# Performance work log

Hardware: AMD Instinct MI355X
Metric: run time of the kernel (lower is better)

## Reference

```python
import jax, jax.numpy as jnp
import numpy as np

HIDDEN = 1024
NUM_HEAD = 16
HEAD_DIM = HIDDEN // NUM_HEAD
B, S = 2, 2048


def setup_inputs() -> dict:
    key = jax.random.key(0)
    ks = jax.random.split(key, 9)
    scale = 1.0 / np.sqrt(HIDDEN)
    X = jax.random.normal(ks[0], (B, S, HIDDEN), dtype=jnp.float32)
    # causal mask, broadcastable over heads: [B, 1, S, S]
    causal = jnp.tril(jnp.ones((S, S), dtype=jnp.int32))
    mask = jnp.broadcast_to(causal[None, None, :, :], (B, 1, S, S))
    Wq = jax.random.normal(ks[1], (HIDDEN, HIDDEN), dtype=jnp.float32) * scale
    bq = jnp.zeros((HIDDEN,), dtype=jnp.float32)
    Wk = jax.random.normal(ks[2], (HIDDEN, HIDDEN), dtype=jnp.float32) * scale
    bk = jnp.zeros((HIDDEN,), dtype=jnp.float32)
    Wv = jax.random.normal(ks[3], (HIDDEN, HIDDEN), dtype=jnp.float32) * scale
    bv = jnp.zeros((HIDDEN,), dtype=jnp.float32)
    Wo = jax.random.normal(ks[4], (HIDDEN, HIDDEN), dtype=jnp.float32) * scale
    bo = jnp.zeros((HIDDEN,), dtype=jnp.float32)
    return {"X": X, "mask": mask, "Wq": Wq, "bq": bq, "Wk": Wk, "bk": bk,
            "Wv": Wv, "bv": bv, "Wo": Wo, "bo": bo}


def reference(X, mask, Wq, bq, Wk, bk, Wv, bv, Wo, bo):
    bsz, seq_len, _ = X.shape
    # Q/K/V projections (torch Linear: x @ W.T + b; here W stored as [in, out])
    Q = X @ Wq + bq
    K = X @ Wk + bk
    V = X @ Wv + bv
    # [B, H, S, D]
    Q = Q.reshape(bsz, seq_len, NUM_HEAD, HEAD_DIM).transpose(0, 2, 1, 3)
    K = K.reshape(bsz, seq_len, NUM_HEAD, HEAD_DIM).transpose(0, 2, 1, 3)
    V = V.reshape(bsz, seq_len, NUM_HEAD, HEAD_DIM).transpose(0, 2, 1, 3)
    # scores: [B, H, S, S]
    scores = jnp.einsum('bhqd,bhkd->bhqk', Q, K) / jnp.sqrt(
        jnp.asarray(HEAD_DIM, dtype=X.dtype))
    scores = jnp.where(mask == 0, jnp.asarray(-jnp.inf, dtype=scores.dtype), scores)
    # dropout (rate=0.0) is identity; softmax over keys
    attn = jax.nn.softmax(scores, axis=-1)
    out = jnp.einsum('bhqk,bhkd->bhqd', attn, V)
    out = out.transpose(0, 2, 1, 3).reshape(bsz, seq_len, HIDDEN)
    return out @ Wo + bo
```

## Files before the change

### kernel.cpp

```cpp
#include <hip/hip_runtime.h>
#include <stdint.h>

#define HID 1024
#define SEQ 2048
#define NB 2
#define NH 16
#define HD 64
#define MROWS 4096

typedef float f32x4 __attribute__((ext_vector_type(4)));
typedef short s16x4 __attribute__((ext_vector_type(4)));
typedef short s16x8 __attribute__((ext_vector_type(8)));

#define MFMA16(a, b, c) __builtin_amdgcn_mfma_f32_16x16x32_bf16((a), (b), (c), 0, 0, 0)

#define GLOAD_LDS16(gp, lp)                                                    \
  __builtin_amdgcn_global_load_lds(                                            \
      (const __attribute__((address_space(1))) unsigned int*)(gp),             \
      (__attribute__((address_space(3))) unsigned int*)(lp), 16, 0, 0)

__device__ __forceinline__ short f2bf(float x) {
  uint32_t u = __builtin_bit_cast(uint32_t, x);
  u += 0x7fffu + ((u >> 16) & 1u);
  return (short)(u >> 16);
}

__global__ __launch_bounds__(256) void cast_x_kernel(const float* __restrict__ src,
                                                     short* __restrict__ dst) {
  const size_t i = (size_t)blockIdx.x * 256 + threadIdx.x;
  const float* s = src + i * 8;
  f32x4 a = *(const f32x4*)(s);
  f32x4 b = *(const f32x4*)(s + 4);
  s16x8 o;
  o[0] = f2bf(a[0]); o[1] = f2bf(a[1]); o[2] = f2bf(a[2]); o[3] = f2bf(a[3]);
  o[4] = f2bf(b[0]); o[5] = f2bf(b[1]); o[6] = f2bf(b[2]); o[7] = f2bf(b[3]);
  *(s16x8*)(dst + i * 8) = o;
}

__global__ __launch_bounds__(256) void transpose_cast4_kernel(
    const float* __restrict__ w0, const float* __restrict__ w1,
    const float* __restrict__ w2, const float* __restrict__ w3,
    short* __restrict__ dstall) {
  __shared__ float t[32][33];
  const int z = blockIdx.z;
  const float* src = (z == 0) ? w0 : (z == 1) ? w1 : (z == 2) ? w2 : w3;
  short* dst = dstall + ((size_t)z << 20);
  const int tx = threadIdx.x & 31, ty = threadIdx.x >> 5;
  const int r0 = blockIdx.y * 32, c0 = blockIdx.x * 32;
#pragma unroll
  for (int i = 0; i < 4; i++)
    t[ty + i * 8][tx] = src[(size_t)(r0 + ty + i * 8) * HID + c0 + tx];
  __syncthreads();
#pragma unroll
  for (int i = 0; i < 4; i++)
    dst[(size_t)(c0 + ty + i * 8) * HID + r0 + tx] = f2bf(t[tx][ty + i * 8]);
}

template <int EPI>
__global__ __launch_bounds__(256) void gemm_bf16(
    const short* __restrict__ A, const short* __restrict__ Bt,
    const float* __restrict__ b0, const float* __restrict__ b1,
    const float* __restrict__ b2, short* __restrict__ Qb, short* __restrict__ Kg,
    short* __restrict__ Vg, float* __restrict__ Out) {
  __shared__ char lds[16384];
  const int tid = threadIdx.x;
  const int w = tid >> 6, l = tid & 63, lg = l >> 4, ln = l & 15;
  const int wm = w >> 1, wn = w & 1;
  const int m0 = blockIdx.y * 128, n0 = blockIdx.x * 128;

  f32x4 acc[4][4];
#pragma unroll
  for (int i = 0; i < 4; i++)
#pragma unroll
    for (int j = 0; j < 4; j++) acc[i][j] = f32x4{0.f, 0.f, 0.f, 0.f};

  for (int k0 = 0; k0 < 1024; k0 += 32) {
    __syncthreads();
#pragma unroll
    for (int i = 0; i < 2; i++) {
      const int chunk = (w * 2 + i) * 64 + l;
      const int row = chunk >> 2;
      const int cs = (chunk & 3) ^ (row & 3);
      GLOAD_LDS16(A + (size_t)(m0 + row) * 1024 + k0 + cs * 8,
                  lds + (w * 2 + i) * 1024);
      GLOAD_LDS16(Bt + (size_t)(n0 + row) * 1024 + k0 + cs * 8,
                  lds + 8192 + (w * 2 + i) * 1024);
    }
    __syncthreads();

    s16x8 af[4], bfr[4];
#pragma unroll
    for (int mi = 0; mi < 4; mi++) {
      const int row = wm * 64 + mi * 16 + ln;
      af[mi] = *(const s16x8*)(lds + row * 64 + ((lg ^ (row & 3)) * 16));
    }
#pragma unroll
    for (int ni = 0; ni < 4; ni++) {
      const int row = wn * 64 + ni * 16 + ln;
      bfr[ni] = *(const s16x8*)(lds + 8192 + row * 64 + ((lg ^ (row & 3)) * 16));
    }
#pragma unroll
    for (int mi = 0; mi < 4; mi++)
#pragma unroll
      for (int ni = 0; ni < 4; ni++)
        acc[mi][ni] = MFMA16(af[mi], bfr[ni], acc[mi][ni]);
  }

#pragma unroll
  for (int ni = 0; ni < 4; ni++) {
    const int c = n0 + wn * 64 + ni * 16 + ln;
    if (EPI == 0) {
      const int mat = c >> 10, cc = c & 1023, hh = cc >> 6, d = cc & 63;
      const float* bp = (mat == 0) ? b0 : (mat == 1) ? b1 : b2;
      const float bias = bp[cc];
#pragma unroll
      for (int mi = 0; mi < 4; mi++) {
#pragma unroll
        for (int r = 0; r < 4; r++) {
          const int m = m0 + wm * 64 + mi * 16 + lg * 4 + r;
          const int bb = m >> 11, s = m & 2047;
          const short v = f2bf(acc[mi][ni][r] + bias);
          const size_t bh = (size_t)(bb * 16 + hh);
          if (mat == 0) {
            Qb[(bh * SEQ + s) * HD + d] = v;
          } else if (mat == 1) {
            const int tile = s >> 6, rr = s & 63;
            Kg[bh * (SEQ * HD) + tile * 4096 + rr * 64 +
               ((((d >> 3) ^ (rr & 7)) << 3) | (d & 7))] = v;
          } else {
            const int sp = (s & ~31) | ((s & 12) << 1) | (((s >> 4) & 1) << 2) |
                           (s & 3);
            const int tile = sp >> 6, kp = sp & 63;
            Vg[bh * (SEQ * HD) + tile * 4096 + d * 64 +
               ((((kp >> 3) ^ (d & 7)) << 3) | (kp & 7))] = v;
          }
        }
      }
    } else {
      const float bias = b0[c];
#pragma unroll
      for (int mi = 0; mi < 4; mi++)
#pragma unroll
        for (int r = 0; r < 4; r++) {
          const int m = m0 + wm * 64 + mi * 16 + lg * 4 + r;
          Out[(size_t)m * 1024 + c] = acc[mi][ni][r] + bias;
        }
    }
  }
}


__device__ __forceinline__ void stage_tile(const short* Kt, const short* Vt,
                                           int t, char* buf, int w, int l) {
  const char* src = (w < 2) ? ((const char*)(Kt + (size_t)t * 4096) + (w & 1) * 4096)
                            : ((const char*)(Vt + (size_t)t * 4096) + (w & 1) * 4096);
  char* dst = buf + ((w < 2) ? 0 : 8192) + (w & 1) * 4096;
#pragma unroll
  for (int j = 0; j < 4; j++)
    GLOAD_LDS16(src + j * 1024 + l * 16, dst + j * 1024);
}

template <bool MASK>
__device__ __forceinline__ void softmax_pv(f32x4 st[4], const s16x8 vf[2][4],
                                           f32x4 o[4], float& m2, float& l_run,
                                           int k0, int qrow, int lg) {
  const float SC = 0.18033688011112042f;
  float p[4][4];
  float pmax = -3e38f;
#pragma unroll
  for (int mt = 0; mt < 4; mt++)
#pragma unroll
    for (int r = 0; r < 4; r++) {
      float v = st[mt][r] * SC;
      if (MASK) {
        const int key = k0 + mt * 16 + lg * 4 + r;
        if (key > qrow) v = -3e38f;
      }
      p[mt][r] = v;
      pmax = fmaxf(pmax, v);
    }
  pmax = fmaxf(pmax, __shfl_xor(pmax, 16));
  pmax = fmaxf(pmax, __shfl_xor(pmax, 32));
  const float m_new = fmaxf(m2, pmax);
  const float corr = exp2f(m2 - m_new);
  float psum = 0.f;
#pragma unroll
  for (int mt = 0; mt < 4; mt++)
#pragma unroll
    for (int r = 0; r < 4; r++) {
      const float e = exp2f(p[mt][r] - m_new);
      p[mt][r] = e;
      psum += e;
    }
  psum += __shfl_xor(psum, 16);
  psum += __shfl_xor(psum, 32);
  l_run = l_run * corr + psum;
  m2 = m_new;
#pragma unroll
  for (int i = 0; i < 4; i++) o[i] *= corr;

  s16x8 pf[2];
#pragma unroll
  for (int s = 0; s < 2; s++)
#pragma unroll
    for (int h = 0; h < 2; h++)
#pragma unroll
      for (int r = 0; r < 4; r++) pf[s][h * 4 + r] = f2bf(p[s * 2 + h][r]);
#pragma unroll
  for (int s = 0; s < 2; s++)
#pragma unroll
    for (int vmt = 0; vmt < 4; vmt++)
      o[vmt] = MFMA16(vf[s][vmt], pf[s], o[vmt]);
}

template <bool MASK>
__device__ __forceinline__ void compute_tile(const char* cbuf, const s16x8& qf0,
                                             const s16x8& qf1, int k0, int qrow,
                                             int lg, int ln, float& m2,
                                             float& l_run, f32x4 o[4]) {
  const int x = ln & 7;
  f32x4 st[4];
#pragma unroll
  for (int mt = 0; mt < 4; mt++) {
    const char* rowp = cbuf + (mt * 16 + ln) * 128;
    const s16x8 k0f = *(const s16x8*)(rowp + ((lg ^ x) * 16));
    const s16x8 k1f = *(const s16x8*)(rowp + (((4 + lg) ^ x) * 16));
    st[mt] = f32x4{0.f, 0.f, 0.f, 0.f};
    st[mt] = MFMA16(k0f, qf0, st[mt]);
    st[mt] = MFMA16(k1f, qf1, st[mt]);
  }
  s16x8 vf[2][4];
#pragma unroll
  for (int s = 0; s < 2; s++)
#pragma unroll
    for (int vmt = 0; vmt < 4; vmt++)
      vf[s][vmt] = *(const s16x8*)(cbuf + 8192 + (vmt * 16 + ln) * 128 +
                                   (((s * 4 + lg) ^ x) * 16));
  softmax_pv<MASK>(st, vf, o, m2, l_run, k0, qrow, lg);
}

__device__ __forceinline__ void attn_group_pass(const short* Kt, const short* Vt,
                                                const short* __restrict__ Qb,
                                                short* __restrict__ Ob, int bh,
                                                int G, int w, int l, char* lds) {
  const int lg = l >> 4, ln = l & 15;
  const int qrow = G * 64 + w * 16 + ln;
  const short* Qp = Qb + ((size_t)bh * SEQ + qrow) * HD;
  const s16x8 qf0 = *(const s16x8*)(Qp + lg * 8);
  const s16x8 qf1 = *(const s16x8*)(Qp + 32 + lg * 8);

  float m2 = -3e38f, l_run = 0.f;
  f32x4 o[4];
#pragma unroll
  for (int i = 0; i < 4; i++) o[i] = f32x4{0.f, 0.f, 0.f, 0.f};

  const int nt = G + 1;
  stage_tile(Kt, Vt, 0, lds, w, l);
  for (int t = 0; t < nt - 1; ++t) {
    stage_tile(Kt, Vt, t + 1, lds + ((t + 1) & 1) * 16384, w, l);
    asm volatile("s_waitcnt vmcnt(4)" ::: "memory");
    __builtin_amdgcn_s_barrier();
    __builtin_amdgcn_sched_barrier(0);
    compute_tile<false>(lds + (t & 1) * 16384, qf0, qf1, t * 64, qrow, lg, ln,
                        m2, l_run, o);
    __builtin_amdgcn_s_barrier();
    __builtin_amdgcn_sched_barrier(0);
  }
  asm volatile("s_waitcnt vmcnt(0)" ::: "memory");
  __builtin_amdgcn_s_barrier();
  __builtin_amdgcn_sched_barrier(0);
  compute_tile<true>(lds + ((nt - 1) & 1) * 16384, qf0, qf1, (nt - 1) * 64, qrow,
                     lg, ln, m2, l_run, o);
  __builtin_amdgcn_s_barrier();
  __builtin_amdgcn_sched_barrier(0);

  const float inv = 1.0f / l_run;
  const int bb = bh >> 4, hh = bh & 15;
  const size_t orow = (size_t)(bb * SEQ + qrow) * HID + hh * HD;
#pragma unroll
  for (int mt = 0; mt < 4; mt++) {
    s16x4 ov;
#pragma unroll
    for (int r = 0; r < 4; r++) ov[r] = f2bf(o[mt][r] * inv);
    *(s16x4*)(Ob + orow + mt * 16 + lg * 4) = ov;
  }
}

__global__ __launch_bounds__(256) void attn_kernel(const short* __restrict__ Qb,
                                                   const short* __restrict__ Kg,
                                                   const short* __restrict__ Vg,
                                                   short* __restrict__ Ob) {
  __shared__ char lds[32768];
  const int bid = blockIdx.x;
  const int L = (bid & 7) * 64 + (bid >> 3);
  const int bh = L >> 4, g = L & 15;
  const int w = threadIdx.x >> 6, l = threadIdx.x & 63;
  const short* Kt = Kg + (size_t)bh * (SEQ * HD);
  const short* Vt = Vg + (size_t)bh * (SEQ * HD);
  attn_group_pass(Kt, Vt, Qb, Ob, bh, g, w, l, lds);
  attn_group_pass(Kt, Vt, Qb, Ob, bh, 31 - g, w, l, lds);
}

extern "C" void kernel_launch(void* const* d_in, const int* in_sizes, int n_in,
                              void* d_out, int out_size, void* d_ws,
                              size_t ws_size, hipStream_t stream) {
  const float* X = (const float*)d_in[0];
  const float* Wq = (const float*)d_in[2];
  const float* bq = (const float*)d_in[3];
  const float* Wk = (const float*)d_in[4];
  const float* bk = (const float*)d_in[5];
  const float* Wv = (const float*)d_in[6];
  const float* bv = (const float*)d_in[7];
  const float* Wo = (const float*)d_in[8];
  const float* bo = (const float*)d_in[9];
  float* out = (float*)d_out;

  char* ws = (char*)d_ws;
  short* Xb = (short*)(ws);
  short* Wtall = (short*)(ws + (8u << 20));
  short* Qb = (short*)(ws + (16u << 20));
  short* Kg = (short*)(ws + (24u << 20));
  short* Vg = (short*)(ws + (32u << 20));
  short* Ob = (short*)(ws + (40u << 20));
  short* Wto = Wtall + (3u << 20);

  cast_x_kernel<<<2048, 256, 0, stream>>>(X, Xb);
  transpose_cast4_kernel<<<dim3(32, 32, 4), 256, 0, stream>>>(Wq, Wk, Wv, Wo,
                                                              Wtall);

  gemm_bf16<0><<<dim3(24, 32), 256, 0, stream>>>(Xb, Wtall, bq, bk, bv, Qb, Kg,
                                                 Vg, nullptr);
  attn_kernel<<<512, 256, 0, stream>>>(Qb, Kg, Vg, Ob);
  gemm_bf16<1><<<dim3(8, 32), 256, 0, stream>>>(Ob, Wto, bo, nullptr, nullptr,
                                                nullptr, nullptr, nullptr, out);
}
```

Measured before the change: 238.0 us.

## Fuse prep kernels, fold softmax scale into Q, lazy rescale, MFMA row-sum

Merges the X cast and weight transpose into one prep launch, applies the softmax scale to Q in the projection epilogue, and skips the online-softmax rescale unless the max grows by more than a threshold. Row sums are computed with an MFMA against a ones vector and P is packed with a packed bf16 convert instruction. The output projection GEMM uses a smaller 64-row tile for a larger grid. Lazy rescaling lets exponent values grow up to 2^8 before correction, and the row sum now uses bf16-rounded probabilities.

```diff
diff --git a/kernel.cpp b/kernel.cpp
--- a/kernel.cpp
+++ b/kernel.cpp
@@ -11,6 +11,7 @@
 typedef float f32x4 __attribute__((ext_vector_type(4)));
 typedef short s16x4 __attribute__((ext_vector_type(4)));
 typedef short s16x8 __attribute__((ext_vector_type(8)));
+typedef uint32_t u32x4 __attribute__((ext_vector_type(4)));
 
 #define MFMA16(a, b, c) __builtin_amdgcn_mfma_f32_16x16x32_bf16((a), (b), (c), 0, 0, 0)
 
@@ -25,26 +26,36 @@
   return (short)(u >> 16);
 }
 
-__global__ __launch_bounds__(256) void cast_x_kernel(const float* __restrict__ src,
-                                                     short* __restrict__ dst) {
-  const size_t i = (size_t)blockIdx.x * 256 + threadIdx.x;
-  const float* s = src + i * 8;
-  f32x4 a = *(const f32x4*)(s);
-  f32x4 b = *(const f32x4*)(s + 4);
-  s16x8 o;
-  o[0] = f2bf(a[0]); o[1] = f2bf(a[1]); o[2] = f2bf(a[2]); o[3] = f2bf(a[3]);
-  o[4] = f2bf(b[0]); o[5] = f2bf(b[1]); o[6] = f2bf(b[2]); o[7] = f2bf(b[3]);
-  *(s16x8*)(dst + i * 8) = o;
-}
-
-__global__ __launch_bounds__(256) void transpose_cast4_kernel(
-    const float* __restrict__ w0, const float* __restrict__ w1,
-    const float* __restrict__ w2, const float* __restrict__ w3,
-    short* __restrict__ dstall) {
+__device__ __forceinline__ uint32_t cvtpk(float lo, float hi) {
+  uint32_t r;
+  asm("v_cvt_pk_bf16_f32 %0, %1, %2" : "=v"(r) : "v"(lo), "v"(hi));
+  return r;
+}
+
+__global__ __launch_bounds__(256) void prep_kernel(
+    const float* __restrict__ X, const float* __restrict__ w0,
+    const float* __restrict__ w1, const float* __restrict__ w2,
+    const float* __restrict__ w3, short* __restrict__ Xb,
+    short* __restrict__ Wtall) {
+  const int z = blockIdx.z;
+  if (z == 4) {
+    const size_t i = ((size_t)blockIdx.y * 32 + blockIdx.x) * 256 + threadIdx.x;
+    const float* s = X + i * 16;
+    short* d = Xb + i * 16;
+#pragma unroll
+    for (int h = 0; h < 2; h++) {
+      f32x4 a = *(const f32x4*)(s + h * 8);
+      f32x4 b = *(const f32x4*)(s + h * 8 + 4);
+      s16x8 o;
+      o[0] = f2bf(a[0]); o[1] = f2bf(a[1]); o[2] = f2bf(a[2]); o[3] = f2bf(a[3]);
+      o[4] = f2bf(b[0]); o[5] = f2bf(b[1]); o[6] = f2bf(b[2]); o[7] = f2bf(b[3]);
+      *(s16x8*)(d + h * 8) = o;
+    }
+    return;
+  }
   __shared__ float t[32][33];
-  const int z = blockIdx.z;
   const float* src = (z == 0) ? w0 : (z == 1) ? w1 : (z == 2) ? w2 : w3;
-  short* dst = dstall + ((size_t)z << 20);
+  short* dst = Wtall + ((size_t)z << 20);
   const int tx = threadIdx.x & 31, ty = threadIdx.x >> 5;
   const int r0 = blockIdx.y * 32, c0 = blockIdx.x * 32;
 #pragma unroll
@@ -56,56 +67,63 @@
     dst[(size_t)(c0 + ty + i * 8) * HID + r0 + tx] = f2bf(t[tx][ty + i * 8]);
 }
 
-template <int EPI>
+template <int EPI, int MI>
 __global__ __launch_bounds__(256) void gemm_bf16(
     const short* __restrict__ A, const short* __restrict__ Bt,
     const float* __restrict__ b0, const float* __restrict__ b1,
     const float* __restrict__ b2, short* __restrict__ Qb, short* __restrict__ Kg,
     short* __restrict__ Vg, float* __restrict__ Out) {
-  __shared__ char lds[16384];
+  __shared__ char lds[MI * 2048 + 8192];
   const int tid = threadIdx.x;
   const int w = tid >> 6, l = tid & 63, lg = l >> 4, ln = l & 15;
   const int wm = w >> 1, wn = w & 1;
-  const int m0 = blockIdx.y * 128, n0 = blockIdx.x * 128;
-
-  f32x4 acc[4][4];
-#pragma unroll
-  for (int i = 0; i < 4; i++)
+  const int m0 = blockIdx.y * (32 * MI), n0 = blockIdx.x * 128;
+
+  f32x4 acc[MI][4];
+#pragma unroll
+  for (int i = 0; i < MI; i++)
 #pragma unroll
     for (int j = 0; j < 4; j++) acc[i][j] = f32x4{0.f, 0.f, 0.f, 0.f};
 
   for (int k0 = 0; k0 < 1024; k0 += 32) {
     __syncthreads();
 #pragma unroll
+    for (int i = 0; i < MI / 2; i++) {
+      const int c = i * 256 + tid;
+      const int row = c >> 2;
+      const int cs = (c & 3) ^ (row & 3);
+      GLOAD_LDS16(A + (size_t)(m0 + row) * 1024 + k0 + cs * 8, lds + c * 16);
+    }
+#pragma unroll
     for (int i = 0; i < 2; i++) {
-      const int chunk = (w * 2 + i) * 64 + l;
-      const int row = chunk >> 2;
-      const int cs = (chunk & 3) ^ (row & 3);
-      GLOAD_LDS16(A + (size_t)(m0 + row) * 1024 + k0 + cs * 8,
-                  lds + (w * 2 + i) * 1024);
+      const int c = i * 256 + tid;
+      const int row = c >> 2;
+      const int cs = (c & 3) ^ (row & 3);
       GLOAD_LDS16(Bt + (size_t)(n0 + row) * 1024 + k0 + cs * 8,
-                  lds + 8192 + (w * 2 + i) * 1024);
+                  lds + MI * 2048 + c * 16);
     }
     __syncthreads();
 
-    s16x8 af[4], bfr[4];
-#pragma unroll
-    for (int mi = 0; mi < 4; mi++) {
-      const int row = wm * 64 + mi * 16 + ln;
+    s16x8 af[MI], bfr[4];
+#pragma unroll
+    for (int mi = 0; mi < MI; mi++) {
+      const int row = wm * (16 * MI) + mi * 16 + ln;
       af[mi] = *(const s16x8*)(lds + row * 64 + ((lg ^ (row & 3)) * 16));
     }
 #pragma unroll
     for (int ni = 0; ni < 4; ni++) {
       const int row = wn * 64 + ni * 16 + ln;
-      bfr[ni] = *(const s16x8*)(lds + 8192 + row * 64 + ((lg ^ (row & 3)) * 16));
-    }
-#pragma unroll
-    for (int mi = 0; mi < 4; mi++)
+      bfr[ni] =
+          *(const s16x8*)(lds + MI * 2048 + row * 64 + ((lg ^ (row & 3)) * 16));
+    }
+#pragma unroll
+    for (int mi = 0; mi < MI; mi++)
 #pragma unroll
       for (int ni = 0; ni < 4; ni++)
         acc[mi][ni] = MFMA16(af[mi], bfr[ni], acc[mi][ni]);
   }
 
+  const float QSC = 0.18033688011112042f;
 #pragma unroll
   for (int ni = 0; ni < 4; ni++) {
     const int c = n0 + wn * 64 + ni * 16 + ln;
@@ -114,35 +132,35 @@
       const float* bp = (mat == 0) ? b0 : (mat == 1) ? b1 : b2;
       const float bias = bp[cc];
 #pragma unroll
-      for (int mi = 0; mi < 4; mi++) {
+      for (int mi = 0; mi < MI; mi++) {
 #pragma unroll
         for (int r = 0; r < 4; r++) {
-          const int m = m0 + wm * 64 + mi * 16 + lg * 4 + r;
+          const int m = m0 + wm * (16 * MI) + mi * 16 + lg * 4 + r;
           const int bb = m >> 11, s = m & 2047;
-          const short v = f2bf(acc[mi][ni][r] + bias);
+          const float fv = acc[mi][ni][r] + bias;
           const size_t bh = (size_t)(bb * 16 + hh);
           if (mat == 0) {
-            Qb[(bh * SEQ + s) * HD + d] = v;
+            Qb[(bh * SEQ + s) * HD + d] = f2bf(fv * QSC);
           } else if (mat == 1) {
             const int tile = s >> 6, rr = s & 63;
             Kg[bh * (SEQ * HD) + tile * 4096 + rr * 64 +
-               ((((d >> 3) ^ (rr & 7)) << 3) | (d & 7))] = v;
+               ((((d >> 3) ^ (rr & 7)) << 3) | (d & 7))] = f2bf(fv);
           } else {
             const int sp = (s & ~31) | ((s & 12) << 1) | (((s >> 4) & 1) << 2) |
                            (s & 3);
             const int tile = sp >> 6, kp = sp & 63;
             Vg[bh * (SEQ * HD) + tile * 4096 + d * 64 +
-               ((((kp >> 3) ^ (d & 7)) << 3) | (kp & 7))] = v;
+               ((((kp >> 3) ^ (d & 7)) << 3) | (kp & 7))] = f2bf(fv);
           }
         }
       }
     } else {
       const float bias = b0[c];
 #pragma unroll
-      for (int mi = 0; mi < 4; mi++)
+      for (int mi = 0; mi < MI; mi++)
 #pragma unroll
         for (int r = 0; r < 4; r++) {
-          const int m = m0 + wm * 64 + mi * 16 + lg * 4 + r;
+          const int m = m0 + wm * (16 * MI) + mi * 16 + lg * 4 + r;
           Out[(size_t)m * 1024 + c] = acc[mi][ni][r] + bias;
         }
     }
@@ -162,62 +180,68 @@
 
 template <bool MASK>
 __device__ __forceinline__ void softmax_pv(f32x4 st[4], const s16x8 vf[2][4],
-                                           f32x4 o[4], float& m2, float& l_run,
-                                           int k0, int qrow, int lg) {
-  const float SC = 0.18033688011112042f;
+                                           const s16x8& ones, f32x4 o[4],
+                                           float& m2, float& l_run, int k0,
+                                           int qrow, int lg) {
   float p[4][4];
-  float pmax = -3e38f;
 #pragma unroll
   for (int mt = 0; mt < 4; mt++)
 #pragma unroll
     for (int r = 0; r < 4; r++) {
-      float v = st[mt][r] * SC;
+      float v = st[mt][r];
       if (MASK) {
         const int key = k0 + mt * 16 + lg * 4 + r;
         if (key > qrow) v = -3e38f;
       }
       p[mt][r] = v;
-      pmax = fmaxf(pmax, v);
-    }
-  pmax = fmaxf(pmax, __shfl_xor(pmax, 16));
-  pmax = fmaxf(pmax, __shfl_xor(pmax, 32));
-  const float m_new = fmaxf(m2, pmax);
-  const float corr = exp2f(m2 - m_new);
-  float psum = 0.f;
+    }
+  float a0 = fmaxf(fmaxf(p[0][0], p[0][1]), fmaxf(p[0][2], p[0][3]));
+  float a1 = fmaxf(fmaxf(p[1][0], p[1][1]), fmaxf(p[1][2], p[1][3]));
+  float a2 = fmaxf(fmaxf(p[2][0], p[2][1]), fmaxf(p[2][2], p[2][3]));
+  float a3 = fmaxf(fmaxf(p[3][0], p[3][1]), fmaxf(p[3][2], p[3][3]));
+  float pmax = fmaxf(fmaxf(a0, a1), fmaxf(a2, a3));
+
+  if (!__all(pmax <= m2 + 8.0f)) {
+    pmax = fmaxf(pmax, __shfl_xor(pmax, 16));
+    pmax = fmaxf(pmax, __shfl_xor(pmax, 32));
+    const float m_new = fmaxf(m2, pmax);
+    const float corr = exp2f(m2 - m_new);
+    l_run *= corr;
+#pragma unroll
+    for (int i = 0; i < 4; i++) o[i] *= corr;
+    m2 = m_new;
+  }
 #pragma unroll
   for (int mt = 0; mt < 4; mt++)
 #pragma unroll
-    for (int r = 0; r < 4; r++) {
-      const float e = exp2f(p[mt][r] - m_new);
-      p[mt][r] = e;
-      psum += e;
-    }
-  psum += __shfl_xor(psum, 16);
-  psum += __shfl_xor(psum, 32);
-  l_run = l_run * corr + psum;
-  m2 = m_new;
-#pragma unroll
-  for (int i = 0; i < 4; i++) o[i] *= corr;
+    for (int r = 0; r < 4; r++) p[mt][r] = exp2f(p[mt][r] - m2);
 
   s16x8 pf[2];
 #pragma unroll
-  for (int s = 0; s < 2; s++)
-#pragma unroll
-    for (int h = 0; h < 2; h++)
-#pragma unroll
-      for (int r = 0; r < 4; r++) pf[s][h * 4 + r] = f2bf(p[s * 2 + h][r]);
+  for (int s = 0; s < 2; s++) {
+    u32x4 wv;
+    wv[0] = cvtpk(p[s * 2][0], p[s * 2][1]);
+    wv[1] = cvtpk(p[s * 2][2], p[s * 2][3]);
+    wv[2] = cvtpk(p[s * 2 + 1][0], p[s * 2 + 1][1]);
+    wv[3] = cvtpk(p[s * 2 + 1][2], p[s * 2 + 1][3]);
+    pf[s] = __builtin_bit_cast(s16x8, wv);
+  }
+  f32x4 ps = f32x4{0.f, 0.f, 0.f, 0.f};
+  ps = MFMA16(ones, pf[0], ps);
+  ps = MFMA16(ones, pf[1], ps);
 #pragma unroll
   for (int s = 0; s < 2; s++)
 #pragma unroll
     for (int vmt = 0; vmt < 4; vmt++)
       o[vmt] = MFMA16(vf[s][vmt], pf[s], o[vmt]);
+  l_run += ps[0];
 }
 
 template <bool MASK>
 __device__ __forceinline__ void compute_tile(const char* cbuf, const s16x8& qf0,
-                                             const s16x8& qf1, int k0, int qrow,
-                                             int lg, int ln, float& m2,
-                                             float& l_run, f32x4 o[4]) {
+                                             const s16x8& qf1, const s16x8& ones,
+                                             int k0, int qrow, int lg, int ln,
+                                             float& m2, float& l_run, f32x4 o[4]) {
   const int x = ln & 7;
   f32x4 st[4];
 #pragma unroll
@@ -236,7 +260,7 @@
     for (int vmt = 0; vmt < 4; vmt++)
       vf[s][vmt] = *(const s16x8*)(cbuf + 8192 + (vmt * 16 + ln) * 128 +
                                    (((s * 4 + lg) ^ x) * 16));
-  softmax_pv<MASK>(st, vf, o, m2, l_run, k0, qrow, lg);
+  softmax_pv<MASK>(st, vf, ones, o, m2, l_run, k0, qrow, lg);
 }
 
 __device__ __forceinline__ void attn_group_pass(const short* Kt, const short* Vt,
@@ -248,6 +272,9 @@
   const short* Qp = Qb + ((size_t)bh * SEQ + qrow) * HD;
   const s16x8 qf0 = *(const s16x8*)(Qp + lg * 8);
   const s16x8 qf1 = *(const s16x8*)(Qp + 32 + lg * 8);
+  s16x8 ones;
+#pragma unroll
+  for (int j = 0; j < 8; j++) ones[j] = (short)0x3F80;
 
   float m2 = -3e38f, l_run = 0.f;
   f32x4 o[4];
@@ -261,16 +288,16 @@
     asm volatile("s_waitcnt vmcnt(4)" ::: "memory");
     __builtin_amdgcn_s_barrier();
     __builtin_amdgcn_sched_barrier(0);
-    compute_tile<false>(lds + (t & 1) * 16384, qf0, qf1, t * 64, qrow, lg, ln,
-                        m2, l_run, o);
+    compute_tile<false>(lds + (t & 1) * 16384, qf0, qf1, ones, t * 64, qrow, lg,
+                        ln, m2, l_run, o);
     __builtin_amdgcn_s_barrier();
     __builtin_amdgcn_sched_barrier(0);
   }
   asm volatile("s_waitcnt vmcnt(0)" ::: "memory");
   __builtin_amdgcn_s_barrier();
   __builtin_amdgcn_sched_barrier(0);
-  compute_tile<true>(lds + ((nt - 1) & 1) * 16384, qf0, qf1, (nt - 1) * 64, qrow,
-                     lg, ln, m2, l_run, o);
+  compute_tile<true>(lds + ((nt - 1) & 1) * 16384, qf0, qf1, ones, (nt - 1) * 64,
+                     qrow, lg, ln, m2, l_run, o);
   __builtin_amdgcn_s_barrier();
   __builtin_amdgcn_sched_barrier(0);
 
@@ -324,13 +351,12 @@
   short* Ob = (short*)(ws + (40u << 20));
   short* Wto = Wtall + (3u << 20);
 
-  cast_x_kernel<<<2048, 256, 0, stream>>>(X, Xb);
-  transpose_cast4_kernel<<<dim3(32, 32, 4), 256, 0, stream>>>(Wq, Wk, Wv, Wo,
-                                                              Wtall);
-
-  gemm_bf16<0><<<dim3(24, 32), 256, 0, stream>>>(Xb, Wtall, bq, bk, bv, Qb, Kg,
-                                                 Vg, nullptr);
+  prep_kernel<<<dim3(32, 32, 5), 256, 0, stream>>>(X, Wq, Wk, Wv, Wo, Xb, Wtall);
+
+  gemm_bf16<0, 4><<<dim3(24, 32), 256, 0, stream>>>(Xb, Wtall, bq, bk, bv, Qb,
+                                                    Kg, Vg, nullptr);
   attn_kernel<<<512, 256, 0, stream>>>(Qb, Kg, Vg, Ob);
-  gemm_bf16<1><<<dim3(8, 32), 256, 0, stream>>>(Ob, Wto, bo, nullptr, nullptr,
-                                                nullptr, nullptr, nullptr, out);
-}
+  gemm_bf16<1, 2><<<dim3(8, 64), 256, 0, stream>>>(Ob, Wto, bo, nullptr, nullptr,
+                                                   nullptr, nullptr, nullptr,
+                                                   out);
+}
```

After: 227.0 us. -4.6%, faster.
